# Kernel optimization log

Measured on AMD Instinct MI355X. Metric: run time of the kernel, lower is better.

Reference implementation:

```python
import jax, jax.numpy as jnp
import numpy as np

# H2RConfig constants
KERNEL = 3
MAX_ROUTES = 1000
STRIDE = 4.0
MIN_SIZE = 32.0
MAX_SIZE = 512.0
SCORE_POWER = 2.0
UNC_WEIGHT = 0.35


def setup_inputs() -> dict:
    key = jax.random.key(0)
    k1, k2, k3 = jax.random.split(key, 3)
    shape = (32, 1, 512, 512)  # [B, 1, H, W] heatmaps at stride 4
    return {
        "route_logits": jax.random.normal(k1, shape, jnp.float32),
        "scale_logits": jax.random.normal(k2, shape, jnp.float32),
        "uncertainty_logits": jax.random.normal(k3, shape, jnp.float32),
        "image_h": 2048,
        "image_w": 2048,
    }


def reference(route_logits, scale_logits, uncertainty_logits, image_h, image_w):
    # score map: sigmoid^power, modulated by uncertainty (use_route_uncertainty=True)
    score = jnp.power(jax.nn.sigmoid(route_logits), SCORE_POWER)
    score = score * (1.0 - UNC_WEIGHT * jax.nn.sigmoid(uncertainty_logits))

    # local-max NMS: 3x3 max pool, stride 1, SAME padding (torch pads with -inf)
    pooled = jax.lax.reduce_window(
        score, -jnp.inf, jax.lax.max,
        window_dimensions=(1, 1, KERNEL, KERNEL),
        window_strides=(1, 1, 1, 1),
        padding="SAME",
    )
    peak_mask = score == pooled
    filtered = jnp.where(peak_mask, score, -1.0)

    B = score.shape[0]
    Wd = score.shape[3]
    flat = filtered.reshape(B, -1)                 # [B, H*W]
    values, indices = jax.lax.top_k(flat, MAX_ROUTES)  # [B, K]
    valid = values > 0.0                            # torch drops these; we mask/pad

    ys = indices // Wd
    xs = indices % Wd
    cx = (xs.astype(jnp.float32) + 0.5) * STRIDE
    cy = (ys.astype(jnp.float32) + 0.5) * STRIDE

    # gather scale / uncertainty at peak locations
    sc = jnp.take_along_axis(scale_logits.reshape(B, -1), indices, axis=1)
    un = jax.nn.sigmoid(jnp.take_along_axis(uncertainty_logits.reshape(B, -1), indices, axis=1))

    side = MIN_SIZE + jax.nn.sigmoid(sc) * (MAX_SIZE - MIN_SIZE)
    side = side * (1.0 + 0.25 * un)
    half = side * 0.5

    iw = float(image_w)
    ih = float(image_h)
    x1 = jnp.clip(cx - half, 0.0, iw - 1.0)
    y1 = jnp.clip(cy - half, 0.0, ih - 1.0)
    x2 = jnp.clip(cx + half, 1.0, iw)
    y2 = jnp.clip(cy + half, 1.0, ih)

    bcol = jnp.broadcast_to(jnp.arange(B, dtype=jnp.float32)[:, None], values.shape)
    rois = jnp.stack([bcol, x1, y1, x2, y2], axis=-1)  # [B, K, 5]

    # padded (fixed-shape) equivalent of torch's variable-length concat
    rois = jnp.where(valid[..., None], rois, 0.0)
    scores = jnp.where(valid, values, 0.0)
    return rois, scores, valid
```

## Files before the change

### kernel.cpp

```cpp
#include <hip/hip_runtime.h>
#include <hip/hip_bf16.h>
#include <math.h>


#define B_   32
#define H_   512
#define W_   512
#define HW_  (H_ * W_)
#define K_   1000
#define ROWS_ 16
#define THR_  512
#define NSTRIP_ 32
#define SEGCAP_ 1200
#define NCLS_ 512
#define CAND4_ 4096

__device__ __forceinline__ int class_of(unsigned int bits) {
    int cls = 2031 - (int)(bits >> 19);
    return cls > (NCLS_ - 1) ? (NCLS_ - 1) : cls;
}

__device__ __forceinline__ float np_expf(float x) {
#pragma clang fp contract(off)
    const float log2e = 1.44269504088896341f;
    float z = x * log2e;
    float m = rintf(z);
    float r = fmaf(m, -0.693359375f, x);
    r = fmaf(m, 2.12194440e-4f, r);
    float r2 = r * r;
    float p = fmaf(1.9875691500e-4f, r, 1.3981999507e-3f);
    p = fmaf(p, r, 8.3334519073e-3f);
    p = fmaf(p, r, 4.1665795894e-2f);
    p = fmaf(p, r, 1.6666665459e-1f);
    p = fmaf(p, r, 5.0000001201e-1f);
    p = fmaf(p, r2, r);
    p = p + 1.0f;
    int mi = (int)m;
    float sc = __int_as_float((127 + mi) << 23);
    return p * sc;
}

__device__ __forceinline__ float sigmoid_np(float x) {
#pragma clang fp contract(off)
    float e = np_expf(-x);
    float d = 1.0f + e;
    return 1.0f / d;
}

__device__ __forceinline__ float score_ref(float r, float u) {
#pragma clang fp contract(off)
    float s  = sigmoid_np(r);
    float s2 = s * s;
    float su = sigmoid_np(u);
    float t  = 0.35f * su;
    float m  = 1.0f - t;
    return s2 * m;
}

__device__ __forceinline__ float sigmoid_fast(float x) {
    return 1.0f / (1.0f + __expf(-x));
}

__global__ __launch_bounds__(THR_, 4) void fused_peak_kernel(
    const float* __restrict__ route, const float* __restrict__ unc,
    unsigned long long* __restrict__ plist, unsigned short* __restrict__ cnt16)
{
    __shared__ float sm[ROWS_ + 2][W_];
    __shared__ unsigned long long pbuf[SEGCAP_];
    __shared__ unsigned int ccnt[NCLS_];
    __shared__ unsigned int coff[NCLS_];
    __shared__ int lcnt;

    const int tid   = threadIdx.x;
    const int lane  = tid & 63;
    const int wid   = tid >> 6;
    const int strip = blockIdx.x;
    const int b     = blockIdx.y;
    const int r0    = strip * ROWS_;
    if (tid == 0) lcnt = 0;
    if (tid < NCLS_) ccnt[tid] = 0u;

    const float4* rb4 = (const float4*)(route + (size_t)b * HW_);
    const float4* ub4 = (const float4*)(unc   + (size_t)b * HW_);
    unsigned long long* seg =
        plist + (size_t)(b * NSTRIP_ + strip) * SEGCAP_;

    float4 rv[5], uv[5];
    int lrow[5], c4[5]; bool ok[5];
    #pragma unroll
    for (int k = 0; k < 5; ++k) {
        int slot = tid + k * THR_;
        slot = slot < 2303 ? slot : 2303;
        int row = slot >> 7;
        int gy  = r0 - 1 + row;
        lrow[k] = row; c4[k] = slot & 127;
        ok[k]   = (gy >= 0 && gy < H_);
        int cy  = gy < 0 ? 0 : (gy >= H_ ? H_ - 1 : gy);
        rv[k] = rb4[cy * 128 + c4[k]];
        uv[k] = ub4[cy * 128 + c4[k]];
    }
    #pragma unroll
    for (int k = 0; k < 5; ++k) {
        float4 s;
        s.x = score_ref(rv[k].x, uv[k].x);
        s.y = score_ref(rv[k].y, uv[k].y);
        s.z = score_ref(rv[k].z, uv[k].z);
        s.w = score_ref(rv[k].w, uv[k].w);
        if (!ok[k]) { s.x = -INFINITY; s.y = -INFINITY;
                      s.z = -INFINITY; s.w = -INFINITY; }
        *(float4*)&sm[lrow[k]][c4[k] * 4] = s;
    }
    __syncthreads();

    #pragma unroll
    for (int j = 0; j < 4; ++j) {
        int g  = tid + j * THR_;
        int ly = 1 + (g >> 7);
        int x0 = (g & 127) * 4;
        int gy = r0 + (ly - 1);
        float4 q0 = *(const float4*)&sm[ly - 1][x0];
        float4 q1 = *(const float4*)&sm[ly    ][x0];
        float4 q2 = *(const float4*)&sm[ly + 1][x0];
        bool hasL = (x0 > 0), hasR = (x0 + 4 < W_);
        float l0 = hasL ? sm[ly - 1][x0 - 1] : -INFINITY;
        float l1 = hasL ? sm[ly    ][x0 - 1] : -INFINITY;
        float l2 = hasL ? sm[ly + 1][x0 - 1] : -INFINITY;
        float e0 = hasR ? sm[ly - 1][x0 + 4] : -INFINITY;
        float e1 = hasR ? sm[ly    ][x0 + 4] : -INFINITY;
        float e2 = hasR ? sm[ly + 1][x0 + 4] : -INFINITY;
        float f_m1 = fmaxf(l0, fmaxf(l1, l2));
        float f_0  = fmaxf(q0.x, fmaxf(q1.x, q2.x));
        float f_1  = fmaxf(q0.y, fmaxf(q1.y, q2.y));
        float f_2  = fmaxf(q0.z, fmaxf(q1.z, q2.z));
        float f_3  = fmaxf(q0.w, fmaxf(q1.w, q2.w));
        float f_4  = fmaxf(e0, fmaxf(e1, e2));
        float tb0  = fmaxf(q0.x, q2.x);
        float tb1  = fmaxf(q0.y, q2.y);
        float tb2  = fmaxf(q0.z, q2.z);
        float tb3  = fmaxf(q0.w, q2.w);
        float vv[4] = { q1.x, q1.y, q1.z, q1.w };
        float mm[4];
        mm[0] = fmaxf(fmaxf(f_m1, f_1), tb0);
        mm[1] = fmaxf(fmaxf(f_0,  f_2), tb1);
        mm[2] = fmaxf(fmaxf(f_1,  f_3), tb2);
        mm[3] = fmaxf(fmaxf(f_2,  f_4), tb3);
        #pragma unroll
        for (int i = 0; i < 4; ++i) {
            bool take = (vv[i] >= mm[i]);
            unsigned long long mk = __ballot(take);
            if (mk) {
                int ldr = __ffsll((unsigned long long)mk) - 1;
                int base_ = 0;
                if (lane == ldr) base_ = atomicAdd(&lcnt, __popcll(mk));
                base_ = __shfl(base_, ldr, 64);
                if (take) {
                    int p = base_ + __popcll(mk & ((1ull << lane) - 1ull));
                    unsigned int bits = __float_as_uint(vv[i]);
                    unsigned int idx  = (unsigned int)(gy * W_ + x0 + i);
                    if (p < SEGCAP_)
                        pbuf[p] = ((unsigned long long)bits << 32)
                                  | (0xFFFFFFFFu - idx);
                }
            }
        }
    }
    __syncthreads();
    const int n = lcnt < SEGCAP_ ? lcnt : SEGCAP_;

    for (int i = tid; i < n; i += THR_)
        atomicAdd(&ccnt[class_of((unsigned int)(pbuf[i] >> 32))], 1u);
    __syncthreads();

    if (wid == 0) {
        int carry = 0;
        for (int k = 0; k < NCLS_ / 64; ++k) {
            int c = k * 64 + lane;
            int v = (int)ccnt[c];
            int pre = v;
            #pragma unroll
            for (int off = 1; off < 64; off <<= 1) {
                int o = __shfl_up(pre, off, 64);
                if (lane >= off) pre += o;
            }
            coff[c] = (unsigned int)(carry + pre - v);
            carry += __shfl(pre, 63, 64);
        }
    }
    __syncthreads();

    for (int i = tid; i < n; i += THR_) {
        unsigned long long key = pbuf[i];
        int cls = class_of((unsigned int)(key >> 32));
        unsigned int pos = atomicAdd(&coff[cls], 1u);
        seg[pos] = key;
    }
    if (tid < NCLS_)
        cnt16[(size_t)(b * NSTRIP_ + strip) * NCLS_ + tid] =
            (unsigned short)ccnt[tid];
}

__global__ __launch_bounds__(1024) void select_kernel(
    const float* __restrict__ scale, const float* __restrict__ unc,
    const unsigned long long* __restrict__ plist,
    const unsigned short* __restrict__ cnt16,
    const int* __restrict__ ih_p, const int* __restrict__ iw_p,
    float* __restrict__ out)
{
    __shared__ __align__(16) unsigned char smem[CAND4_ * 8];
    __shared__ unsigned int tot[NCLS_];
    __shared__ int slen[NSTRIP_], sbase[NSTRIP_];
    __shared__ int sh_C, sh_n;

    unsigned int* scnt = (unsigned int*)smem;
    unsigned long long* cand = (unsigned long long*)smem;

    const int b = blockIdx.x, tid = threadIdx.x;
    const int lane = tid & 63, wid = tid >> 6;
    if (tid == 0) { sh_C = NCLS_ - 1; sh_n = 0; }

    const unsigned int* g =
        (const unsigned int*)(cnt16 + (size_t)b * NSTRIP_ * NCLS_);
    for (int i = tid; i < NSTRIP_ * NCLS_ / 2; i += 1024) scnt[i] = g[i];
    __syncthreads();

    if (tid < NCLS_) {
        unsigned int s = 0;
        for (int st = 0; st < NSTRIP_; ++st) {
            unsigned int w = scnt[st * (NCLS_ / 2) + (tid >> 1)];
            s += (tid & 1) ? (w >> 16) : (w & 0xFFFFu);
        }
        tot[tid] = s;
    }
    __syncthreads();

    if (wid == 0) {
        int cum = 0;
        for (int k = 0; k < NCLS_ / 64; ++k) {
            int c = k * 64 + lane;
            int v = (int)tot[c];
            int pre = v;
            #pragma unroll
            for (int off = 1; off < 64; off <<= 1) {
                int o = __shfl_up(pre, off, 64);
                if (lane >= off) pre += o;
            }
            int ctot = __shfl(pre, 63, 64);
            if (cum + ctot < K_) { cum += ctot; continue; }
            bool cond = (cum + pre) >= K_;
            unsigned long long mask = __ballot(cond);
            int fs = __ffsll((unsigned long long)mask) - 1;
            if (lane == 0) sh_C = k * 64 + fs;
            break;
        }
    }
    __syncthreads();
    const int Cstar = sh_C;

    if (tid < NSTRIP_) {
        int len = 0;
        for (int c = 0; c <= Cstar; ++c) {
            unsigned int w = scnt[tid * (NCLS_ / 2) + (c >> 1)];
            len += (c & 1) ? (int)(w >> 16) : (int)(w & 0xFFFFu);
        }
        slen[tid] = len;
    }
    __syncthreads();
    if (tid == 0) {
        int acc = 0;
        for (int s = 0; s < NSTRIP_; ++s) { sbase[s] = acc; acc += slen[s]; }
        sh_n = acc;
    }
    __syncthreads();

    const int n = sh_n < CAND4_ ? sh_n : CAND4_;
    for (int s = 0; s < NSTRIP_; ++s) {
        int len = slen[s], base = sbase[s];
        const unsigned long long* sg =
            plist + (size_t)(b * NSTRIP_ + s) * SEGCAP_;
        for (int i = tid; i < len; i += 1024)
            if (base + i < CAND4_) cand[base + i] = sg[i];
    }
    __syncthreads();
    int sortN = (n <= 1024) ? 1024 : ((n <= 2048) ? 2048 : CAND4_);
    for (int i = tid; i < sortN; i += 1024)
        if (i >= n) cand[i] = 0ull;

    for (int kk = 2; kk <= sortN; kk <<= 1) {
        for (int jj = kk >> 1; jj > 0; jj >>= 1) {
            __syncthreads();
            for (int p = tid; p < (sortN >> 1); p += 1024) {
                int i   = ((p & ~(jj - 1)) << 1) | (p & (jj - 1));
                int ixj = i | jj;
                bool desc = ((i & kk) == 0);
                unsigned long long a = cand[i], c2 = cand[ixj];
                if (desc ? (a < c2) : (a > c2)) { cand[i] = c2; cand[ixj] = a; }
            }
        }
    }
    __syncthreads();

    const float fih = (float)(*ih_p);
    const float fiw = (float)(*iw_p);
    float* rois   = out;
    float* scores = out + (size_t)B_ * K_ * 5;
    float* validf = out + (size_t)B_ * K_ * 6;

    for (int k = tid; k < K_; k += 1024) {
        int o = b * K_ + k;
        unsigned long long key = cand[k];
        unsigned int bits = (unsigned int)(key >> 32);
        if (bits == 0u) {
            rois[o * 5 + 0] = 0.0f; rois[o * 5 + 1] = 0.0f;
            rois[o * 5 + 2] = 0.0f; rois[o * 5 + 3] = 0.0f;
            rois[o * 5 + 4] = 0.0f;
            scores[o] = 0.0f; validf[o] = 0.0f;
        } else {
            float v = __uint_as_float(bits);
            unsigned int idx = 0xFFFFFFFFu - (unsigned int)(key & 0xFFFFFFFFull);
            int y = (int)(idx >> 9), x = (int)(idx & 511u);
            float cx = ((float)x + 0.5f) * 4.0f;
            float cy = ((float)y + 0.5f) * 4.0f;
            float ss = sigmoid_fast(scale[(size_t)b * HW_ + idx]);
            float su = sigmoid_fast(unc  [(size_t)b * HW_ + idx]);
            float side = (32.0f + ss * 480.0f) * (1.0f + 0.25f * su);
            float half = 0.5f * side;
            float x1 = fminf(fmaxf(cx - half, 0.0f), fiw - 1.0f);
            float y1 = fminf(fmaxf(cy - half, 0.0f), fih - 1.0f);
            float x2 = fminf(fmaxf(cx + half, 1.0f), fiw);
            float y2 = fminf(fmaxf(cy + half, 1.0f), fih);
            rois[o * 5 + 0] = (float)b;
            rois[o * 5 + 1] = x1; rois[o * 5 + 2] = y1;
            rois[o * 5 + 3] = x2; rois[o * 5 + 4] = y2;
            scores[o] = v; validf[o] = 1.0f;
        }
    }
}

extern "C" void kernel_launch(void* const* d_in, const int* in_sizes, int n_in,
                              void* d_out, int out_size, void* d_ws, size_t ws_size,
                              hipStream_t stream) {
    const float* route = (const float*)d_in[0];
    const float* scale = (const float*)d_in[1];
    const float* unc   = (const float*)d_in[2];
    const int*   ih    = (const int*)d_in[3];
    const int*   iw    = (const int*)d_in[4];
    float* out = (float*)d_out;

    unsigned short* cnt16 = (unsigned short*)d_ws;
    unsigned long long* plist =
        (unsigned long long*)((char*)d_ws + (size_t)B_ * NSTRIP_ * NCLS_ * 2);

    dim3 g(NSTRIP_, B_);
    fused_peak_kernel<<<g, THR_, 0, stream>>>(route, unc, plist, cnt16);
    select_kernel<<<B_, 1024, 0, stream>>>(scale, unc, plist, cnt16,
                                           ih, iw, out);
}
```

Baseline: 170.4 us.

## Refine boundary class with second-level histogram to shrink bitonic sort size

The select kernel now splits candidates into those strictly above the threshold class and those in the boundary class. When the combined set is large, it builds a finer 12-bit histogram over the boundary-class keys, picks a secondary threshold, and compacts only the needed keys into a 2048-entry buffer. This caps the bitonic sort at 2048 elements instead of up to 4096, cutting sort passes. The cost is an extra histogram pass, ballot-based compaction and more shared memory, and candidates above the cap may be dropped if the bucket counts are skewed.

```diff
diff --git a/kernel.cpp b/kernel.cpp
--- a/kernel.cpp
+++ b/kernel.cpp
@@ -13,7 +13,8 @@
 #define NSTRIP_ 32
 #define SEGCAP_ 1200
 #define NCLS_ 512
-#define CAND4_ 4096
+#define CROSSCAP_ 4096
+#define CANDCAP_ 2048
 
 __device__ __forceinline__ int class_of(unsigned int bits) {
     int cls = 2031 - (int)(bits >> 19);
@@ -206,17 +207,20 @@
     const int* __restrict__ ih_p, const int* __restrict__ iw_p,
     float* __restrict__ out)
 {
-    __shared__ __align__(16) unsigned char smem[CAND4_ * 8];
+    __shared__ __align__(16) unsigned char scr[32768];
+    __shared__ unsigned long long cand[CANDCAP_];
+    __shared__ unsigned int hist[2048];
     __shared__ unsigned int tot[NCLS_];
-    __shared__ int slen[NSTRIP_], sbase[NSTRIP_];
-    __shared__ int sh_C, sh_n;
-
-    unsigned int* scnt = (unsigned int*)smem;
-    unsigned long long* cand = (unsigned long long*)smem;
+    __shared__ int slenA[NSTRIP_], sbaseA[NSTRIP_];
+    __shared__ int slenC[NSTRIP_], sbaseC[NSTRIP_];
+    __shared__ int sh_C, sh_A, sh_ncross, sh_T2, sh_nsel;
+
+    unsigned int* scnt = (unsigned int*)scr;
+    unsigned long long* cross = (unsigned long long*)scr;
 
     const int b = blockIdx.x, tid = threadIdx.x;
     const int lane = tid & 63, wid = tid >> 6;
-    if (tid == 0) { sh_C = NCLS_ - 1; sh_n = 0; }
+    if (tid == 0) { sh_C = NCLS_ - 1; sh_A = 0; sh_T2 = 0; }
 
     const unsigned int* g =
         (const unsigned int*)(cnt16 + (size_t)b * NSTRIP_ * NCLS_);
@@ -249,41 +253,117 @@
             bool cond = (cum + pre) >= K_;
             unsigned long long mask = __ballot(cond);
             int fs = __ffsll((unsigned long long)mask) - 1;
-            if (lane == 0) sh_C = k * 64 + fs;
+            int pres = __shfl(pre, fs, 64);
+            int vs   = __shfl(v, fs, 64);
+            if (lane == 0) { sh_C = k * 64 + fs; sh_A = cum + pres - vs; }
             break;
         }
     }
     __syncthreads();
-    const int Cstar = sh_C;
+    const int Cstar = sh_C, A = sh_A;
 
     if (tid < NSTRIP_) {
-        int len = 0;
-        for (int c = 0; c <= Cstar; ++c) {
+        int lenA = 0;
+        for (int c = 0; c < Cstar; ++c) {
             unsigned int w = scnt[tid * (NCLS_ / 2) + (c >> 1)];
-            len += (c & 1) ? (int)(w >> 16) : (int)(w & 0xFFFFu);
-        }
-        slen[tid] = len;
+            lenA += (c & 1) ? (int)(w >> 16) : (int)(w & 0xFFFFu);
+        }
+        unsigned int wc = scnt[tid * (NCLS_ / 2) + (Cstar >> 1)];
+        slenA[tid] = lenA;
+        slenC[tid] = (Cstar & 1) ? (int)(wc >> 16) : (int)(wc & 0xFFFFu);
     }
     __syncthreads();
     if (tid == 0) {
-        int acc = 0;
-        for (int s = 0; s < NSTRIP_; ++s) { sbase[s] = acc; acc += slen[s]; }
-        sh_n = acc;
-    }
-    __syncthreads();
-
-    const int n = sh_n < CAND4_ ? sh_n : CAND4_;
-    for (int s = 0; s < NSTRIP_; ++s) {
-        int len = slen[s], base = sbase[s];
+        int aA = 0, aC = 0;
+        for (int s = 0; s < NSTRIP_; ++s) {
+            sbaseA[s] = aA; aA += slenA[s];
+            sbaseC[s] = aC; aC += slenC[s];
+        }
+        sh_ncross = aC;
+    }
+    __syncthreads();
+    const int ncross = sh_ncross < CROSSCAP_ ? sh_ncross : CROSSCAP_;
+    const bool simple = (A + ncross) <= CANDCAP_ / 2;
+    __syncthreads();
+
+    for (int s = wid; s < NSTRIP_; s += 16) {
+        int lenA = slenA[s], baseA = sbaseA[s];
+        int lenC = slenC[s], baseC = sbaseC[s];
         const unsigned long long* sg =
             plist + (size_t)(b * NSTRIP_ + s) * SEGCAP_;
-        for (int i = tid; i < len; i += 1024)
-            if (base + i < CAND4_) cand[base + i] = sg[i];
-    }
-    __syncthreads();
-    int sortN = (n <= 1024) ? 1024 : ((n <= 2048) ? 2048 : CAND4_);
+        for (int i = lane; i < lenA; i += 64)
+            cand[baseA + i] = sg[i];
+        if (simple) {
+            for (int i = lane; i < lenC; i += 64)
+                cand[A + baseC + i] = sg[lenA + i];
+        } else {
+            for (int i = lane; i < lenC; i += 64)
+                if (baseC + i < CROSSCAP_) cross[baseC + i] = sg[lenA + i];
+        }
+    }
+
+    int nsel;
+    if (simple) {
+        nsel = A + ncross;
+        __syncthreads();
+    } else {
+        for (int i = tid; i < 2048; i += 1024) hist[i] = 0u;
+        __syncthreads();
+        for (int i = tid; i < ncross; i += 1024) {
+            unsigned int sb = ((unsigned int)(cross[i] >> 39)) & 0xFFFu;
+            atomicAdd(&hist[sb >> 1], 1u << ((sb & 1) * 16));
+        }
+        __syncthreads();
+        if (wid == 0) {
+            int cum = 0;
+            for (int k = 63; k >= 0; --k) {
+                int bucket = k * 64 + lane;
+                int cnt = (int)((hist[bucket >> 1] >> ((bucket & 1) * 16))
+                                & 0xFFFFu);
+                int sum = cnt;
+                #pragma unroll
+                for (int off = 32; off > 0; off >>= 1)
+                    sum += __shfl_down(sum, off, 64);
+                sum = __shfl(sum, 0, 64);
+                if (A + cum + sum < K_) { cum += sum; continue; }
+                int suf = cnt;
+                #pragma unroll
+                for (int off = 1; off < 64; off <<= 1) {
+                    int o = __shfl_down(suf, off, 64);
+                    suf += (lane + off < 64) ? o : 0;
+                }
+                bool cond = (A + cum + suf) >= K_;
+                unsigned long long mask = __ballot(cond);
+                int ls = 63 - __builtin_clzll(mask);
+                if (lane == 0) sh_T2 = k * 64 + ls;
+                break;
+            }
+        }
+        if (tid == 0) sh_nsel = A;
+        __syncthreads();
+        const unsigned int T2 = (unsigned int)sh_T2;
+        for (int i = tid; i < ncross; i += 1024) {
+            unsigned long long key = cross[i];
+            bool take = ((((unsigned int)(key >> 39))) & 0xFFFu) >= T2;
+            unsigned long long mk = __ballot(take);
+            if (mk) {
+                int ldr = __ffsll((unsigned long long)mk) - 1;
+                int base_ = 0;
+                if (lane == ldr) base_ = atomicAdd(&sh_nsel, __popcll(mk));
+                base_ = __shfl(base_, ldr, 64);
+                if (take) {
+                    int p = base_ + __popcll(mk & ((1ull << lane) - 1ull));
+                    if (p < CANDCAP_) cand[p] = key;
+                }
+            }
+        }
+        __syncthreads();
+        nsel = sh_nsel < CANDCAP_ ? sh_nsel : CANDCAP_;
+    }
+
+    int sortN = (nsel <= 1024) ? 1024 : CANDCAP_;
     for (int i = tid; i < sortN; i += 1024)
-        if (i >= n) cand[i] = 0ull;
+        if (i >= nsel) cand[i] = 0ull;
 
     for (int kk = 2; kk <= sortN; kk <<= 1) {
         for (int jj = kk >> 1; jj > 0; jj >>= 1) {
```

After: 172.2 us. Within noise of the previous version (+1.0%).
